# Kernel optimization log

Hardware: AMD Instinct MI355X
Metric: run time of the kernel (lower is better)

The kernel has to match this reference:

```python
import jax, jax.numpy as jnp
import numpy as np

N_NODES = 50000
N_EDGES = 800000


def gcn_conv(x, W, b, row, col, n):
    # PyG GCNConv: x' = D^-1/2 (A+I) D^-1/2 (x W) + b, flow source->target
    h = x @ W  # [N, out]
    # add self loops
    loop = jnp.arange(n, dtype=row.dtype)
    r = jnp.concatenate([row, loop])
    c = jnp.concatenate([col, loop])
    deg = jax.ops.segment_sum(jnp.ones_like(c, dtype=h.dtype), c, num_segments=n)
    dinv = jnp.where(deg > 0, jax.lax.rsqrt(deg), 0.0)
    norm = dinv[r] * dinv[c]  # [E+N]
    msg = h[r] * norm[:, None]  # gather + scale
    out = jax.ops.segment_sum(msg, c, num_segments=n)  # scatter-add
    return out + b


def setup_inputs() -> dict:
    key = jax.random.key(0)
    ks = jax.random.split(key, 6)
    F_in, H = 128, 128
    x = jax.random.normal(ks[0], (N_NODES, F_in), dtype=jnp.float32)
    edge_index = jax.random.randint(ks[1], (2, N_EDGES), 0, N_NODES, dtype=jnp.int64)
    s1 = 1.0 / np.sqrt(F_in)
    s2 = 1.0 / np.sqrt(H)
    return {
        "x": x,
        "edge_index": edge_index,
        "W1": jax.random.normal(ks[2], (F_in, H), dtype=jnp.float32) * s1,
        "b1": jnp.zeros((H,), dtype=jnp.float32),
        "W2": jax.random.normal(ks[3], (H, H), dtype=jnp.float32) * s2,
        "b2": jnp.zeros((H,), dtype=jnp.float32),
        "W3": jax.random.normal(ks[4], (H, 1), dtype=jnp.float32) * s2,
        "b3": jnp.zeros((1,), dtype=jnp.float32),
    }


def reference(x, edge_index, W1, b1, W2, b2, W3, b3):
    n = x.shape[0]
    row, col = edge_index[0], edge_index[1]
    # dropout is identity in eval mode (F.dropout training=False)
    h = gcn_conv(x, W1, b1, row, col, n)
    h = jax.nn.relu(h)
    h = gcn_conv(h, W2, b2, row, col, n)
    h = jax.nn.relu(h)
    out = gcn_conv(h, W3, b3, row, col, n)  # [N, 1]
    return out
```

## Files before the change

kernel.cpp:

```cpp
#include <hip/hip_runtime.h>
#include <hip/hip_fp16.h>


typedef float nfloat4 __attribute__((ext_vector_type(4)));

__global__ __launch_bounds__(256) void k_prep(const int* __restrict__ ei,
                                              int* __restrict__ cnt, int* __restrict__ ctr,
                                              int E, int N) {
  int e = blockIdx.x * 256 + threadIdx.x;
  if (e == 0) __hip_atomic_store(ctr, 0, __ATOMIC_RELAXED, __HIP_MEMORY_SCOPE_AGENT);
  if (e < E) {
    unsigned c = (unsigned)ei[E + e];
    if (c < (unsigned)N) atomicAdd(&cnt[c], 1);
  }
}

__global__ __launch_bounds__(256) void k_scan(const int* __restrict__ cnt, int* __restrict__ offs,
                                              int* __restrict__ cursor, float* __restrict__ dinv,
                                              int* __restrict__ gsum, int* __restrict__ ctr,
                                              int N, int E, int NB) {
  __shared__ int s[256];
  int tid = threadIdx.x, b = blockIdx.x;
  int i = b * 256 + tid;
  int v = (i < N) ? cnt[i] : 0;
  if (i < N) dinv[i] = rsqrtf((float)(v + 1));
  s[tid] = v;
  __syncthreads();
  for (int d = 1; d < 256; d <<= 1) {
    int t = (tid >= d) ? s[tid - d] : 0;
    __syncthreads();
    s[tid] += t;
    __syncthreads();
  }
  int lexcl = s[tid] - v;
  if (tid == 0) {
    __hip_atomic_store(&gsum[b], s[255], __ATOMIC_RELEASE, __HIP_MEMORY_SCOPE_AGENT);
    __hip_atomic_fetch_add(ctr, 1, __ATOMIC_ACQ_REL, __HIP_MEMORY_SCOPE_AGENT);
    while (__hip_atomic_load(ctr, __ATOMIC_ACQUIRE, __HIP_MEMORY_SCOPE_AGENT) < NB)
      __builtin_amdgcn_s_sleep(8);
  }
  __syncthreads();
  int part = (tid < b) ? __hip_atomic_load(&gsum[tid], __ATOMIC_RELAXED, __HIP_MEMORY_SCOPE_AGENT) : 0;
  s[tid] = part;
  __syncthreads();
  for (int d = 128; d > 0; d >>= 1) {
    if (tid < d) s[tid] += s[tid + d];
    __syncthreads();
  }
  int o = s[0] + lexcl;
  if (i < N) {
    offs[i] = o;
    cursor[i] = o;
  }
  if (i == 0) offs[N] = E;
}

__global__ __launch_bounds__(256) void k_fill(const int* __restrict__ ei,
                                              int* __restrict__ cursor, int* __restrict__ csr_src,
                                              int E, int N) {
  int s = blockIdx.x & 7;
  int chunk = blockIdx.x >> 3;
  int e = chunk * 256 + threadIdx.x;
  unsigned lo = (unsigned)((s * (long long)N) >> 3);
  unsigned hi = (unsigned)(((s + 1) * (long long)N) >> 3);
  if (e < E) {
    unsigned c = (unsigned)ei[E + e];
    if (c >= lo && c < hi) {
      unsigned r = (unsigned)ei[e];
      if (r < (unsigned)N) {
        int p = atomicAdd(&cursor[c], 1);
        csr_src[p] = (int)r;
      }
    }
  }
}

__global__ __launch_bounds__(512) void k_gemm(const float* __restrict__ X, const float* __restrict__ W,
                                              const float* __restrict__ dinv, __half* __restrict__ G,
                                              int N) {
  __shared__ float Wl[32 * 128];
  int tid = threadIdx.x;
  int row0 = blockIdx.x * 64;
  int cg = tid & 31;
  int rg = tid >> 5;
  const float4* __restrict__ X4 = (const float4*)X;

  size_t xb[4];
#pragma unroll
  for (int r = 0; r < 4; r++) {
    int grow = row0 + rg * 4 + r;
    xb[r] = (size_t)((grow < N) ? grow : (N - 1)) * 32;
  }

  float acc[4][4];
#pragma unroll
  for (int a = 0; a < 4; a++)
#pragma unroll
    for (int b = 0; b < 4; b++) acc[a][b] = 0.f;

  for (int kt = 0; kt < 4; kt++) {
    __syncthreads();
    for (int i = tid; i < 1024; i += 512)
      ((float4*)Wl)[i] = ((const float4*)W)[kt * 1024 + i];
    __syncthreads();
#pragma unroll
    for (int k4 = 0; k4 < 8; k4++) {
      float4 wv[4];
#pragma unroll
      for (int kk = 0; kk < 4; kk++)
        wv[kk] = ((const float4*)(Wl + (k4 * 4 + kk) * 128))[cg];
#pragma unroll
      for (int r = 0; r < 4; r++) {
        float4 xv = X4[xb[r] + kt * 8 + k4];
        acc[r][0] = fmaf(xv.x, wv[0].x, acc[r][0]);
        acc[r][1] = fmaf(xv.x, wv[0].y, acc[r][1]);
        acc[r][2] = fmaf(xv.x, wv[0].z, acc[r][2]);
        acc[r][3] = fmaf(xv.x, wv[0].w, acc[r][3]);
        acc[r][0] = fmaf(xv.y, wv[1].x, acc[r][0]);
        acc[r][1] = fmaf(xv.y, wv[1].y, acc[r][1]);
        acc[r][2] = fmaf(xv.y, wv[1].z, acc[r][2]);
        acc[r][3] = fmaf(xv.y, wv[1].w, acc[r][3]);
        acc[r][0] = fmaf(xv.z, wv[2].x, acc[r][0]);
        acc[r][1] = fmaf(xv.z, wv[2].y, acc[r][1]);
        acc[r][2] = fmaf(xv.z, wv[2].z, acc[r][2]);
        acc[r][3] = fmaf(xv.z, wv[2].w, acc[r][3]);
        acc[r][0] = fmaf(xv.w, wv[3].x, acc[r][0]);
        acc[r][1] = fmaf(xv.w, wv[3].y, acc[r][1]);
        acc[r][2] = fmaf(xv.w, wv[3].z, acc[r][2]);
        acc[r][3] = fmaf(xv.w, wv[3].w, acc[r][3]);
      }
    }
  }

#pragma unroll
  for (int ri = 0; ri < 4; ri++) {
    int grow = row0 + rg * 4 + ri;
    if (grow < N) {
      float di = dinv[grow];
      __half2 h0 = __floats2half2_rn(di * acc[ri][0], di * acc[ri][1]);
      __half2 h1 = __floats2half2_rn(di * acc[ri][2], di * acc[ri][3]);
      uint2 u;
      u.x = *reinterpret_cast<unsigned*>(&h0);
      u.y = *reinterpret_cast<unsigned*>(&h1);
      ((uint2*)G)[(size_t)grow * 32 + cg] = u;
    }
  }
}

__device__ inline float4 cvt4(uint2 u) {
  __half2 a = *reinterpret_cast<__half2*>(&u.x);
  __half2 b = *reinterpret_cast<__half2*>(&u.y);
  float2 fa = __half22float2(a);
  float2 fb = __half22float2(b);
  return make_float4(fa.x, fa.y, fb.x, fb.y);
}

__global__ __launch_bounds__(256) void k_agg(const __half* __restrict__ g, const int* __restrict__ offs,
                                             const int* __restrict__ csr, const float* __restrict__ dinv,
                                             const float* __restrict__ bias, float* __restrict__ t, int N) {
  int v = blockIdx.x * 4 + (threadIdx.x >> 6);
  if (v >= N) return;
  int lane = threadIdx.x & 63;
  int half = lane >> 5;
  int fc = lane & 31;
  const uint2* __restrict__ G2 = (const uint2*)g;

  float4 a0 = make_float4(0.f, 0.f, 0.f, 0.f);
  float4 a1 = make_float4(0.f, 0.f, 0.f, 0.f);
  if (half == 0) a0 = cvt4(G2[(size_t)v * 32 + fc]);

  int s0 = offs[v], s1 = offs[v + 1];
  int i = s0 + half;
  for (; i + 6 < s1; i += 8) {
    int e0 = csr[i];
    int e1 = csr[i + 2];
    int e2 = csr[i + 4];
    int e3 = csr[i + 6];
    uint2 r0 = G2[(size_t)e0 * 32 + fc];
    uint2 r1 = G2[(size_t)e1 * 32 + fc];
    uint2 r2 = G2[(size_t)e2 * 32 + fc];
    uint2 r3 = G2[(size_t)e3 * 32 + fc];
    float4 f0 = cvt4(r0), f1 = cvt4(r1), f2 = cvt4(r2), f3 = cvt4(r3);
    a0.x += f0.x; a0.y += f0.y; a0.z += f0.z; a0.w += f0.w;
    a1.x += f1.x; a1.y += f1.y; a1.z += f1.z; a1.w += f1.w;
    a0.x += f2.x; a0.y += f2.y; a0.z += f2.z; a0.w += f2.w;
    a1.x += f3.x; a1.y += f3.y; a1.z += f3.z; a1.w += f3.w;
  }
  for (; i < s1; i += 2) {
    float4 f = cvt4(G2[(size_t)csr[i] * 32 + fc]);
    a0.x += f.x; a0.y += f.y; a0.z += f.z; a0.w += f.w;
  }
  a0.x += a1.x; a0.y += a1.y; a0.z += a1.z; a0.w += a1.w;

  a0.x += __shfl_xor(a0.x, 32, 64);
  a0.y += __shfl_xor(a0.y, 32, 64);
  a0.z += __shfl_xor(a0.z, 32, 64);
  a0.w += __shfl_xor(a0.w, 32, 64);

  if (half == 0) {
    float di = dinv[v];
    float4 bb = ((const float4*)bias)[fc];
    float4 o;
    o.x = fmaxf(fmaf(di, a0.x, bb.x), 0.f);
    o.y = fmaxf(fmaf(di, a0.y, bb.y), 0.f);
    o.z = fmaxf(fmaf(di, a0.z, bb.z), 0.f);
    o.w = fmaxf(fmaf(di, a0.w, bb.w), 0.f);
    ((float4*)t)[(size_t)v * 32 + fc] = o;
  }
}

__global__ __launch_bounds__(256) void k_gemv3(const float* __restrict__ t2, const float* __restrict__ W3,
                                               const float* __restrict__ dinv, float* __restrict__ g3, int N) {
  int wave = threadIdx.x >> 6;
  int lane = threadIdx.x & 63;
  int r = blockIdx.x * 4 + wave;
  if (r >= N) return;
  float2 xv = ((const float2*)t2)[(size_t)r * 64 + lane];
  float2 wv = ((const float2*)W3)[lane];
  float s = xv.x * wv.x + xv.y * wv.y;
  for (int d = 32; d > 0; d >>= 1) s += __shfl_down(s, d, 64);
  if (lane == 0) g3[r] = dinv[r] * s;
}

__global__ __launch_bounds__(256) void k_agg3(const float* __restrict__ g3, const int* __restrict__ offs,
                                              const int* __restrict__ csr_src, const float* __restrict__ dinv,
                                              const float* __restrict__ b3, float* __restrict__ out, int N) {
  int v = blockIdx.x * 256 + threadIdx.x;
  if (v < N) {
    float acc = g3[v];
    int i = offs[v], s1 = offs[v + 1];
    for (; i + 3 < s1; i += 4) {
      int e0 = csr_src[i], e1 = csr_src[i + 1], e2 = csr_src[i + 2], e3 = csr_src[i + 3];
      float r0 = g3[e0], r1 = g3[e1], r2 = g3[e2], r3 = g3[e3];
      acc += r0 + r1 + r2 + r3;
    }
    for (; i < s1; i++) acc += g3[csr_src[i]];
    out[v] = dinv[v] * acc + b3[0];
  }
}

extern "C" void kernel_launch(void* const* d_in, const int* in_sizes, int n_in,
                              void* d_out, int out_size, void* d_ws, size_t ws_size,
                              hipStream_t stream) {
  const float* x = (const float*)d_in[0];
  const int* ei = (const int*)d_in[1];
  const float* W1 = (const float*)d_in[2];
  const float* b1 = (const float*)d_in[3];
  const float* W2 = (const float*)d_in[4];
  const float* b2 = (const float*)d_in[5];
  const float* W3 = (const float*)d_in[6];
  const float* b3 = (const float*)d_in[7];
  float* out = (float*)d_out;

  int N = in_sizes[0] / 128;
  int E = in_sizes[1] / 2;

  char* base = (char*)d_ws;
  size_t off = 0;
  auto alloc = [&](size_t bytes) -> void* {
    void* p = base + off;
    off += (bytes + 255) & ~(size_t)255;
    return p;
  };
  int* cnt = (int*)alloc((size_t)N * 4);
  int* offs = (int*)alloc(((size_t)N + 1) * 4);
  int* cursor = (int*)alloc((size_t)N * 4);
  int* csr = (int*)alloc((size_t)E * 4);
  float* dinv = (float*)alloc((size_t)N * 4);
  int* gsum = (int*)alloc(4096 * 4);
  int* ctr = (int*)alloc(256);
  __half* gH = (__half*)alloc((size_t)N * 128 * 2);
  float* tA = (float*)alloc((size_t)N * 128 * 4);
  float* g3 = (float*)alloc((size_t)N * 4);
  (void)ws_size;

  (void)hipMemsetAsync(cnt, 0, (size_t)N * 4, stream);

  int gE = (E + 255) / 256;
  int gN = (N + 255) / 256;
  k_prep<<<gE, 256, 0, stream>>>(ei, cnt, ctr, E, N);
  k_scan<<<gN, 256, 0, stream>>>(cnt, offs, cursor, dinv, gsum, ctr, N, E, gN);
  k_fill<<<8 * gE, 256, 0, stream>>>(ei, cursor, csr, E, N);

  int gG = (N + 63) / 64;
  int gA = (N + 3) / 4;
  k_gemm<<<gG, 512, 0, stream>>>(x, W1, dinv, gH, N);
  k_agg<<<gA, 256, 0, stream>>>(gH, offs, csr, dinv, b1, tA, N);
  k_gemm<<<gG, 512, 0, stream>>>(tA, W2, dinv, gH, N);
  k_agg<<<gA, 256, 0, stream>>>(gH, offs, csr, dinv, b2, tA, N);
  k_gemv3<<<gA, 256, 0, stream>>>(tA, W3, dinv, g3, N);
  k_agg3<<<gN, 256, 0, stream>>>(g3, offs, csr, dinv, b3, out, N);
}
```

Measured before the change: 336.6 us.

## Use fp16 MFMA for dense layers with pre-transposed swizzled weights

Replaces the scalar FP32 FMA GEMM with a kernel built on 16x16x32 fp16 MFMA instructions. Weights W1/W2 are converted to fp16 once, transposed, and XOR-swizzled into workspace inside the scan kernel, so each GEMM block loads the whole 128x128 tile into LDS without bank conflicts. Activations are converted to fp16 on the fly, which costs some input precision. The aim is to cut GEMM compute time, which is a modest share next to the gather-bound aggregation kernels.

Result: faster. 280.5 us (-16.7%).

```diff
diff --git a/kernel.cpp b/kernel.cpp
--- a/kernel.cpp
+++ b/kernel.cpp
@@ -3,6 +3,8 @@
 
 
 typedef float nfloat4 __attribute__((ext_vector_type(4)));
+typedef _Float16 half8 __attribute__((ext_vector_type(8)));
+typedef float f32x4 __attribute__((ext_vector_type(4)));
 
 __global__ __launch_bounds__(256) void k_prep(const int* __restrict__ ei,
                                               int* __restrict__ cnt, int* __restrict__ ctr,
@@ -18,10 +20,22 @@
 __global__ __launch_bounds__(256) void k_scan(const int* __restrict__ cnt, int* __restrict__ offs,
                                               int* __restrict__ cursor, float* __restrict__ dinv,
                                               int* __restrict__ gsum, int* __restrict__ ctr,
+                                              const float* __restrict__ W1, const float* __restrict__ W2,
+                                              _Float16* __restrict__ WtA, _Float16* __restrict__ WtB,
                                               int N, int E, int NB) {
   __shared__ int s[256];
   int tid = threadIdx.x, b = blockIdx.x;
   int i = b * 256 + tid;
+
+  if (i < 32768) {
+    int which = i >> 14, e = i & 16383;
+    int c = e >> 7, k = e & 127;
+    const float* Wsrc = which ? W2 : W1;
+    _Float16 h = (_Float16)Wsrc[k * 128 + c];
+    char* dst = (char*)(which ? WtB : WtA);
+    *(_Float16*)(dst + c * 256 + ((k * 2) ^ ((c & 7) << 4))) = h;
+  }
+
   int v = (i < N) ? cnt[i] : 0;
   if (i < N) dinv[i] = rsqrtf((float)(v + 1));
   s[tid] = v;
@@ -75,74 +89,61 @@
   }
 }
 
-__global__ __launch_bounds__(512) void k_gemm(const float* __restrict__ X, const float* __restrict__ W,
-                                              const float* __restrict__ dinv, __half* __restrict__ G,
-                                              int N) {
-  __shared__ float Wl[32 * 128];
+__global__ __launch_bounds__(256) void k_gemm(const float* __restrict__ X,
+                                              const _Float16* __restrict__ Wt,
+                                              const float* __restrict__ dinv,
+                                              __half* __restrict__ G, int N) {
+  __shared__ _Float16 Wl[128 * 128];
   int tid = threadIdx.x;
-  int row0 = blockIdx.x * 64;
-  int cg = tid & 31;
-  int rg = tid >> 5;
+  int w = tid >> 6;
+  int l = tid & 63;
+  int cl = l & 15;
+  int kg = l >> 4;
+  int row0 = blockIdx.x * 64 + w * 16;
+
+  for (int i = tid; i < 2048; i += 256)
+    ((uint4*)Wl)[i] = ((const uint4*)Wt)[i];
+  __syncthreads();
+
+  int ra = row0 + cl;
+  size_t xb = (size_t)((ra < N) ? ra : (N - 1)) * 32;
   const float4* __restrict__ X4 = (const float4*)X;
-
-  size_t xb[4];
+  half8 a[4];
+#pragma unroll
+  for (int k0 = 0; k0 < 4; k0++) {
+    float4 f0 = X4[xb + k0 * 8 + kg * 2];
+    float4 f1 = X4[xb + k0 * 8 + kg * 2 + 1];
+    half8 h;
+    h[0] = (_Float16)f0.x; h[1] = (_Float16)f0.y;
+    h[2] = (_Float16)f0.z; h[3] = (_Float16)f0.w;
+    h[4] = (_Float16)f1.x; h[5] = (_Float16)f1.y;
+    h[6] = (_Float16)f1.z; h[7] = (_Float16)f1.w;
+    a[k0] = h;
+  }
+
+  int rowc = row0 + kg * 4;
+  float dv[4];
 #pragma unroll
   for (int r = 0; r < 4; r++) {
-    int grow = row0 + rg * 4 + r;
-    xb[r] = (size_t)((grow < N) ? grow : (N - 1)) * 32;
-  }
-
-  float acc[4][4];
-#pragma unroll
-  for (int a = 0; a < 4; a++)
-#pragma unroll
-    for (int b = 0; b < 4; b++) acc[a][b] = 0.f;
-
-  for (int kt = 0; kt < 4; kt++) {
-    __syncthreads();
-    for (int i = tid; i < 1024; i += 512)
-      ((float4*)Wl)[i] = ((const float4*)W)[kt * 1024 + i];
-    __syncthreads();
-#pragma unroll
-    for (int k4 = 0; k4 < 8; k4++) {
-      float4 wv[4];
-#pragma unroll
-      for (int kk = 0; kk < 4; kk++)
-        wv[kk] = ((const float4*)(Wl + (k4 * 4 + kk) * 128))[cg];
-#pragma unroll
-      for (int r = 0; r < 4; r++) {
-        float4 xv = X4[xb[r] + kt * 8 + k4];
-        acc[r][0] = fmaf(xv.x, wv[0].x, acc[r][0]);
-        acc[r][1] = fmaf(xv.x, wv[0].y, acc[r][1]);
-        acc[r][2] = fmaf(xv.x, wv[0].z, acc[r][2]);
-        acc[r][3] = fmaf(xv.x, wv[0].w, acc[r][3]);
-        acc[r][0] = fmaf(xv.y, wv[1].x, acc[r][0]);
-        acc[r][1] = fmaf(xv.y, wv[1].y, acc[r][1]);
-        acc[r][2] = fmaf(xv.y, wv[1].z, acc[r][2]);
-        acc[r][3] = fmaf(xv.y, wv[1].w, acc[r][3]);
-        acc[r][0] = fmaf(xv.z, wv[2].x, acc[r][0]);
-        acc[r][1] = fmaf(xv.z, wv[2].y, acc[r][1]);
-        acc[r][2] = fmaf(xv.z, wv[2].z, acc[r][2]);
-        acc[r][3] = fmaf(xv.z, wv[2].w, acc[r][3]);
-        acc[r][0] = fmaf(xv.w, wv[3].x, acc[r][0]);
-        acc[r][1] = fmaf(xv.w, wv[3].y, acc[r][1]);
-        acc[r][2] = fmaf(xv.w, wv[3].z, acc[r][2]);
-        acc[r][3] = fmaf(xv.w, wv[3].w, acc[r][3]);
-      }
-    }
-  }
-
-#pragma unroll
-  for (int ri = 0; ri < 4; ri++) {
-    int grow = row0 + rg * 4 + ri;
-    if (grow < N) {
-      float di = dinv[grow];
-      __half2 h0 = __floats2half2_rn(di * acc[ri][0], di * acc[ri][1]);
-      __half2 h1 = __floats2half2_rn(di * acc[ri][2], di * acc[ri][3]);
-      uint2 u;
-      u.x = *reinterpret_cast<unsigned*>(&h0);
-      u.y = *reinterpret_cast<unsigned*>(&h1);
-      ((uint2*)G)[(size_t)grow * 32 + cg] = u;
+    int rc = rowc + r;
+    dv[r] = dinv[(rc < N) ? rc : (N - 1)];
+  }
+
+#pragma unroll
+  for (int g = 0; g < 8; g++) {
+    int col = g * 16 + cl;
+    int swz = (col & 7) << 4;
+    f32x4 acc = {0.f, 0.f, 0.f, 0.f};
+#pragma unroll
+    for (int k0 = 0; k0 < 4; k0++) {
+      int byteoff = col * 256 + ((k0 * 64 + kg * 16) ^ swz);
+      half8 bfrag = *(const half8*)((const char*)Wl + byteoff);
+      acc = __builtin_amdgcn_mfma_f32_16x16x32_f16(a[k0], bfrag, acc, 0, 0, 0);
+    }
+#pragma unroll
+    for (int r = 0; r < 4; r++) {
+      int rc = rowc + r;
+      if (rc < N) G[(size_t)rc * 128 + g * 16 + cl] = __float2half_rn(dv[r] * acc[r]);
     }
   }
 }
@@ -269,6 +270,8 @@
   float* dinv = (float*)alloc((size_t)N * 4);
   int* gsum = (int*)alloc(4096 * 4);
   int* ctr = (int*)alloc(256);
+  _Float16* WtA = (_Float16*)alloc(128 * 128 * 2);
+  _Float16* WtB = (_Float16*)alloc(128 * 128 * 2);
   __half* gH = (__half*)alloc((size_t)N * 128 * 2);
   float* tA = (float*)alloc((size_t)N * 128 * 4);
   float* g3 = (float*)alloc((size_t)N * 4);
@@ -279,14 +282,14 @@
   int gE = (E + 255) / 256;
   int gN = (N + 255) / 256;
   k_prep<<<gE, 256, 0, stream>>>(ei, cnt, ctr, E, N);
-  k_scan<<<gN, 256, 0, stream>>>(cnt, offs, cursor, dinv, gsum, ctr, N, E, gN);
+  k_scan<<<gN, 256, 0, stream>>>(cnt, offs, cursor, dinv, gsum, ctr, W1, W2, WtA, WtB, N, E, gN);
   k_fill<<<8 * gE, 256, 0, stream>>>(ei, cursor, csr, E, N);
 
   int gG = (N + 63) / 64;
   int gA = (N + 3) / 4;
-  k_gemm<<<gG, 512, 0, stream>>>(x, W1, dinv, gH, N);
+  k_gemm<<<gG, 256, 0, stream>>>(x, WtA, dinv, gH, N);
   k_agg<<<gA, 256, 0, stream>>>(gH, offs, csr, dinv, b1, tA, N);
-  k_gemm<<<gG, 512, 0, stream>>>(tA, W2, dinv, gH, N);
+  k_gemm<<<gG, 256, 0, stream>>>(tA, WtB, dinv, gH, N);
   k_agg<<<gA, 256, 0, stream>>>(gH, offs, csr, dinv, b2, tA, N);
   k_gemv3<<<gA, 256, 0, stream>>>(tA, W3, dinv, g3, N);
   k_agg3<<<gN, 256, 0, stream>>>(g3, offs, csr, dinv, b3, out, N);
```
